# Performance work log

Measured on AMD Instinct MI355X. Metric: run time of the kernel, lower is better.

## Reference

```python
import jax, jax.numpy as jnp
import numpy as np

COST_CLASS = 1.0
COST_BBOX = 5.0
COST_GIOU = 2.0
EPS = 1e-7


def box_cxcywh_to_xyxy(x):
    cx, cy, w, h = x[..., 0], x[..., 1], x[..., 2], x[..., 3]
    return jnp.stack([cx - 0.5 * w, cy - 0.5 * h, cx + 0.5 * w, cy + 0.5 * h], axis=-1)


def generalized_box_iou(boxes1, boxes2):
    # boxes1: [N,4] xyxy, boxes2: [M,4] xyxy -> [N,M]
    area1 = (boxes1[:, 2] - boxes1[:, 0]) * (boxes1[:, 3] - boxes1[:, 1])
    area2 = (boxes2[:, 2] - boxes2[:, 0]) * (boxes2[:, 3] - boxes2[:, 1])
    lt = jnp.maximum(boxes1[:, None, :2], boxes2[None, :, :2])
    rb = jnp.minimum(boxes1[:, None, 2:], boxes2[None, :, 2:])
    wh = jnp.clip(rb - lt, 0.0)
    inter = wh[..., 0] * wh[..., 1]
    union = area1[:, None] + area2[None, :] - inter
    iou = inter / (union + EPS)
    # smallest enclosing box
    lt_c = jnp.minimum(boxes1[:, None, :2], boxes2[None, :, :2])
    rb_c = jnp.maximum(boxes1[:, None, 2:], boxes2[None, :, 2:])
    wh_c = jnp.clip(rb_c - lt_c, 0.0)
    c_area = wh_c[..., 0] * wh_c[..., 1]
    return iou - (c_area - union) / (c_area + EPS)


def setup_inputs() -> dict:
    key = jax.random.key(0)
    k1, k2, k3, k4 = jax.random.split(key, 4)
    bs, nq, nc, nt = 16, 900, 256, 800
    pred_logits = jax.random.normal(k1, (bs, nq, nc), dtype=jnp.float32)
    pred_boxes = jax.random.uniform(k2, (bs, nq, 4), dtype=jnp.float32)
    tgt_labels = jax.random.randint(k3, (nt,), 0, nc, dtype=jnp.int64)
    tgt_boxes = jax.random.uniform(k4, (nt, 4), dtype=jnp.float32)
    return {"pred_logits": pred_logits, "pred_boxes": pred_boxes,
            "tgt_labels": tgt_labels, "tgt_boxes": tgt_boxes}


def reference(pred_logits, pred_boxes, tgt_labels, tgt_boxes):
    # Returns the full pairwise matching cost tensor C: [bs, num_queries, total_targets].
    # (The scipy linear_sum_assignment / CPU Hungarian step consumes this on host.)
    bs, nq, nc = pred_logits.shape
    out_prob = jax.nn.softmax(pred_logits.reshape(bs * nq, nc), axis=-1)  # [N, nc]
    out_bbox = pred_boxes.reshape(bs * nq, 4)                              # [N, 4]
    cost_class = -out_prob[:, tgt_labels]                                  # [N, M]
    cost_bbox = jnp.abs(out_bbox[:, None, :] - tgt_boxes[None, :, :]).sum(-1)  # L1 cdist [N, M]
    cost_giou = -generalized_box_iou(box_cxcywh_to_xyxy(out_bbox),
                                     box_cxcywh_to_xyxy(tgt_boxes))        # [N, M]
    C = COST_BBOX * cost_bbox + COST_CLASS * cost_class + COST_GIOU * cost_giou
    return C.reshape(bs, nq, -1)
```

## Files before the change

kernel.cpp:

```cpp
#include <hip/hip_runtime.h>
#include <hip/hip_bf16.h>


constexpr float EPS = 1e-7f;

__device__ __forceinline__ float pair_cost(
    const float4& pb, float ax1, float ay1, float ax2, float ay2, float area1,
    const float4& tb, float prob)
{
    const float l1 = fabsf(pb.x - tb.x) + fabsf(pb.y - tb.y)
                   + fabsf(pb.z - tb.z) + fabsf(pb.w - tb.w);

    const float bx1 = tb.x - 0.5f * tb.z, by1 = tb.y - 0.5f * tb.w;
    const float bx2 = tb.x + 0.5f * tb.z, by2 = tb.y + 0.5f * tb.w;
    const float area2 = tb.z * tb.w;

    const float iw = fmaxf(fminf(ax2, bx2) - fmaxf(ax1, bx1), 0.0f);
    const float ih = fmaxf(fminf(ay2, by2) - fmaxf(ay1, by1), 0.0f);
    const float inter = iw * ih;
    const float uni   = area1 + area2 - inter;
    const float iou   = inter * __builtin_amdgcn_rcpf(uni + EPS);

    const float cw = fmaxf(ax2, bx2) - fminf(ax1, bx1);
    const float ch = fmaxf(ay2, by2) - fminf(ay1, by1);
    const float carea = cw * ch;

    const float giou = iou - (carea - uni) * __builtin_amdgcn_rcpf(carea + EPS);
    return 5.0f * l1 - prob - 2.0f * giou;
}

__global__ __launch_bounds__(256) void matcher_opt(
    const float* __restrict__ logits,
    const float* __restrict__ pboxes,
    const int*   __restrict__ labels,
    const float* __restrict__ tboxes,
    float* __restrict__ out,
    int N)
{
    const int wave = threadIdx.x >> 6;
    const int lane = threadIdx.x & 63;

    __shared__ float4 s_tb[800];
    __shared__ int    s_lb[800];
    __shared__ float  s_prob[4][256];

    for (int i = threadIdx.x; i < 800; i += 256) {
        s_tb[i] = reinterpret_cast<const float4*>(tboxes)[i];
        s_lb[i] = labels[i] & 255;
    }
    __syncthreads();

    float* sp = s_prob[wave];

    const int n0 = (blockIdx.x * 4 + wave) * 4;
    #pragma unroll 1
    for (int r = 0; r < 4; ++r) {
        const int n = n0 + r;
        if (n >= N) return;

        const float4 lg =
            reinterpret_cast<const float4*>(logits)[(size_t)n * 64 + lane];
        float mx = fmaxf(fmaxf(lg.x, lg.y), fmaxf(lg.z, lg.w));
        #pragma unroll
        for (int off = 32; off > 0; off >>= 1)
            mx = fmaxf(mx, __shfl_xor(mx, off, 64));
        const float e0 = __expf(lg.x - mx), e1 = __expf(lg.y - mx);
        const float e2 = __expf(lg.z - mx), e3 = __expf(lg.w - mx);
        float s = (e0 + e1) + (e2 + e3);
        #pragma unroll
        for (int off = 32; off > 0; off >>= 1)
            s += __shfl_xor(s, off, 64);
        const float inv = __builtin_amdgcn_rcpf(s);
        reinterpret_cast<float4*>(sp)[lane] =
            make_float4(e0 * inv, e1 * inv, e2 * inv, e3 * inv);

        const float4 pb = reinterpret_cast<const float4*>(pboxes)[n];
        const float ax1 = pb.x - 0.5f * pb.z, ay1 = pb.y - 0.5f * pb.w;
        const float ax2 = pb.x + 0.5f * pb.z, ay2 = pb.y + 0.5f * pb.w;
        const float area1 = pb.z * pb.w;

        float* orow = out + (size_t)n * 800;

        #pragma unroll 4
        for (int m = lane; m < 768; m += 64) {
            const float4 tb = s_tb[m];
            orow[m] = pair_cost(pb, ax1, ay1, ax2, ay2, area1, tb, sp[s_lb[m]]);
        }
        if (lane < 32) {
            const int m = 768 + lane;
            orow[m] = pair_cost(pb, ax1, ay1, ax2, ay2, area1, s_tb[m],
                                sp[s_lb[m]]);
        }
    }
}

__global__ __launch_bounds__(256) void matcher_generic(
    const float* __restrict__ logits, const float* __restrict__ pboxes,
    const int* __restrict__ labels, const float* __restrict__ tboxes,
    float* __restrict__ out, int N, int M, int NC, int lbl_mask)
{
    const int wave = threadIdx.x >> 6;
    const int lane = threadIdx.x & 63;
    const int n    = blockIdx.x * 4 + wave;

    extern __shared__ float s_dyn[];
    float* sp = s_dyn + wave * NC;

    if (n < N) {
        float mx = -3.4e38f;
        for (int c = lane; c < NC; c += 64) mx = fmaxf(mx, logits[(size_t)n * NC + c]);
        #pragma unroll
        for (int off = 32; off > 0; off >>= 1) mx = fmaxf(mx, __shfl_xor(mx, off, 64));
        float s = 0.f;
        for (int c = lane; c < NC; c += 64) {
            const float e = __expf(logits[(size_t)n * NC + c] - mx);
            sp[c] = e; s += e;
        }
        #pragma unroll
        for (int off = 32; off > 0; off >>= 1) s += __shfl_xor(s, off, 64);
        const float inv = __builtin_amdgcn_rcpf(s);
        for (int c = lane; c < NC; c += 64) sp[c] *= inv;
    }
    __syncthreads();
    if (n >= N) return;

    const float4 pb = reinterpret_cast<const float4*>(pboxes)[n];
    const float ax1 = pb.x - 0.5f * pb.z, ay1 = pb.y - 0.5f * pb.w;
    const float ax2 = pb.x + 0.5f * pb.z, ay2 = pb.y + 0.5f * pb.w;
    const float area1 = pb.z * pb.w;
    float* orow = out + (size_t)n * M;

    for (int m = lane; m < M; m += 64) {
        const float4 tb = reinterpret_cast<const float4*>(tboxes)[m];
        orow[m] = pair_cost(pb, ax1, ay1, ax2, ay2, area1, tb,
                            sp[labels[m] & lbl_mask]);
    }
}

extern "C" void kernel_launch(void* const* d_in, const int* in_sizes, int n_in,
                              void* d_out, int out_size, void* d_ws, size_t ws_size,
                              hipStream_t stream) {
    const float* logits = (const float*)d_in[0];
    const float* pboxes = (const float*)d_in[1];
    const int*   labels = (const int*)d_in[2];
    const float* tboxes = (const float*)d_in[3];

    const int N  = in_sizes[1] / 4;
    const int M  = in_sizes[2];
    const int NC = in_sizes[0] / N;

    if (NC == 256 && M == 800) {
        const int waves = (N + 3) / 4;
        const int grid  = (waves + 3) / 4;
        matcher_opt<<<grid, 256, 0, stream>>>(
            logits, pboxes, labels, tboxes, (float*)d_out, N);
    } else {
        int lbl_mask = 1; while (lbl_mask < NC) lbl_mask <<= 1;
        --lbl_mask;
        const int grid = (N + 3) / 4;
        matcher_generic<<<grid, 256, 4 * NC * sizeof(float), stream>>>(
            logits, pboxes, labels, tboxes, (float*)d_out, N, M, NC, lbl_mask);
    }
}
```

Measured before the change: 93.46 us.

## Process two query rows per wave with shared target-box preprocessing and nontemporal stores

Each wave now handles two query rows together instead of looping over four rows. Target-box corner and area values are computed once and reused for both rows, and the two softmax reductions are interleaved. Logits and prediction boxes are loaded before the shared-memory fill so the global load latency overlaps it. Output is written with nontemporal stores and the grid is doubled, which means more blocks each repeat the 800-entry target table load into shared memory.

```diff
diff --git a/kernel.cpp b/kernel.cpp
--- a/kernel.cpp
+++ b/kernel.cpp
@@ -4,16 +4,13 @@
 
 constexpr float EPS = 1e-7f;
 
-__device__ __forceinline__ float pair_cost(
+__device__ __forceinline__ float pair_cost_pp(
     const float4& pb, float ax1, float ay1, float ax2, float ay2, float area1,
-    const float4& tb, float prob)
+    const float4& tb, float bx1, float by1, float bx2, float by2, float area2,
+    float prob)
 {
     const float l1 = fabsf(pb.x - tb.x) + fabsf(pb.y - tb.y)
                    + fabsf(pb.z - tb.z) + fabsf(pb.w - tb.w);
-
-    const float bx1 = tb.x - 0.5f * tb.z, by1 = tb.y - 0.5f * tb.w;
-    const float bx2 = tb.x + 0.5f * tb.z, by2 = tb.y + 0.5f * tb.w;
-    const float area2 = tb.z * tb.w;
 
     const float iw = fmaxf(fminf(ax2, bx2) - fmaxf(ax1, bx1), 0.0f);
     const float ih = fmaxf(fminf(ay2, by2) - fmaxf(ay1, by1), 0.0f);
@@ -42,55 +39,98 @@
 
     __shared__ float4 s_tb[800];
     __shared__ int    s_lb[800];
-    __shared__ float  s_prob[4][256];
+    __shared__ float  s_prob[8][256];
+
+    const int n0 = (blockIdx.x * 4 + wave) * 2;
+    const int n1 = n0 + 1;
+    const bool v0 = n0 < N;
+    const bool v1 = n1 < N;
+
+    float4 lg0 = make_float4(0, 0, 0, 0), lg1 = lg0;
+    float4 pb0 = make_float4(0, 0, 0, 0), pb1 = pb0;
+    if (v0) {
+        lg0 = reinterpret_cast<const float4*>(logits)[(size_t)n0 * 64 + lane];
+        pb0 = reinterpret_cast<const float4*>(pboxes)[n0];
+    }
+    if (v1) {
+        lg1 = reinterpret_cast<const float4*>(logits)[(size_t)n1 * 64 + lane];
+        pb1 = reinterpret_cast<const float4*>(pboxes)[n1];
+    }
 
     for (int i = threadIdx.x; i < 800; i += 256) {
         s_tb[i] = reinterpret_cast<const float4*>(tboxes)[i];
         s_lb[i] = labels[i] & 255;
     }
     __syncthreads();
-
-    float* sp = s_prob[wave];
-
-    const int n0 = (blockIdx.x * 4 + wave) * 4;
-    #pragma unroll 1
-    for (int r = 0; r < 4; ++r) {
-        const int n = n0 + r;
-        if (n >= N) return;
-
-        const float4 lg =
-            reinterpret_cast<const float4*>(logits)[(size_t)n * 64 + lane];
-        float mx = fmaxf(fmaxf(lg.x, lg.y), fmaxf(lg.z, lg.w));
-        #pragma unroll
-        for (int off = 32; off > 0; off >>= 1)
-            mx = fmaxf(mx, __shfl_xor(mx, off, 64));
-        const float e0 = __expf(lg.x - mx), e1 = __expf(lg.y - mx);
-        const float e2 = __expf(lg.z - mx), e3 = __expf(lg.w - mx);
-        float s = (e0 + e1) + (e2 + e3);
-        #pragma unroll
-        for (int off = 32; off > 0; off >>= 1)
-            s += __shfl_xor(s, off, 64);
-        const float inv = __builtin_amdgcn_rcpf(s);
-        reinterpret_cast<float4*>(sp)[lane] =
-            make_float4(e0 * inv, e1 * inv, e2 * inv, e3 * inv);
-
-        const float4 pb = reinterpret_cast<const float4*>(pboxes)[n];
-        const float ax1 = pb.x - 0.5f * pb.z, ay1 = pb.y - 0.5f * pb.w;
-        const float ax2 = pb.x + 0.5f * pb.z, ay2 = pb.y + 0.5f * pb.w;
-        const float area1 = pb.z * pb.w;
-
-        float* orow = out + (size_t)n * 800;
-
-        #pragma unroll 4
-        for (int m = lane; m < 768; m += 64) {
-            const float4 tb = s_tb[m];
-            orow[m] = pair_cost(pb, ax1, ay1, ax2, ay2, area1, tb, sp[s_lb[m]]);
-        }
-        if (lane < 32) {
-            const int m = 768 + lane;
-            orow[m] = pair_cost(pb, ax1, ay1, ax2, ay2, area1, s_tb[m],
-                                sp[s_lb[m]]);
-        }
+    if (!v0) return;
+    if (!v1) { lg1 = lg0; pb1 = pb0; }
+
+    float mx0 = fmaxf(fmaxf(lg0.x, lg0.y), fmaxf(lg0.z, lg0.w));
+    float mx1 = fmaxf(fmaxf(lg1.x, lg1.y), fmaxf(lg1.z, lg1.w));
+    #pragma unroll
+    for (int off = 32; off > 0; off >>= 1) {
+        mx0 = fmaxf(mx0, __shfl_xor(mx0, off, 64));
+        mx1 = fmaxf(mx1, __shfl_xor(mx1, off, 64));
+    }
+    const float e00 = __expf(lg0.x - mx0), e01 = __expf(lg0.y - mx0);
+    const float e02 = __expf(lg0.z - mx0), e03 = __expf(lg0.w - mx0);
+    const float e10 = __expf(lg1.x - mx1), e11 = __expf(lg1.y - mx1);
+    const float e12 = __expf(lg1.z - mx1), e13 = __expf(lg1.w - mx1);
+    float s0 = (e00 + e01) + (e02 + e03);
+    float s1 = (e10 + e11) + (e12 + e13);
+    #pragma unroll
+    for (int off = 32; off > 0; off >>= 1) {
+        s0 += __shfl_xor(s0, off, 64);
+        s1 += __shfl_xor(s1, off, 64);
+    }
+    const float inv0 = __builtin_amdgcn_rcpf(s0);
+    const float inv1 = __builtin_amdgcn_rcpf(s1);
+    float* sp0 = s_prob[wave * 2 + 0];
+    float* sp1 = s_prob[wave * 2 + 1];
+    reinterpret_cast<float4*>(sp0)[lane] =
+        make_float4(e00 * inv0, e01 * inv0, e02 * inv0, e03 * inv0);
+    reinterpret_cast<float4*>(sp1)[lane] =
+        make_float4(e10 * inv1, e11 * inv1, e12 * inv1, e13 * inv1);
+
+    const float ax10 = pb0.x - 0.5f * pb0.z, ay10 = pb0.y - 0.5f * pb0.w;
+    const float ax20 = pb0.x + 0.5f * pb0.z, ay20 = pb0.y + 0.5f * pb0.w;
+    const float area10 = pb0.z * pb0.w;
+    const float ax11 = pb1.x - 0.5f * pb1.z, ay11 = pb1.y - 0.5f * pb1.w;
+    const float ax21 = pb1.x + 0.5f * pb1.z, ay21 = pb1.y + 0.5f * pb1.w;
+    const float area11 = pb1.z * pb1.w;
+
+    float* orow0 = out + (size_t)n0 * 800;
+    float* orow1 = v1 ? out + (size_t)n1 * 800 : orow0;
+
+    #pragma unroll 2
+    for (int m = lane; m < 768; m += 64) {
+        const float4 tb = s_tb[m];
+        const int   lbl = s_lb[m];
+        const float p0  = sp0[lbl];
+        const float p1  = sp1[lbl];
+        const float bx1 = tb.x - 0.5f * tb.z, by1 = tb.y - 0.5f * tb.w;
+        const float bx2 = tb.x + 0.5f * tb.z, by2 = tb.y + 0.5f * tb.w;
+        const float area2 = tb.z * tb.w;
+        const float c0 = pair_cost_pp(pb0, ax10, ay10, ax20, ay20, area10,
+                                      tb, bx1, by1, bx2, by2, area2, p0);
+        const float c1 = pair_cost_pp(pb1, ax11, ay11, ax21, ay21, area11,
+                                      tb, bx1, by1, bx2, by2, area2, p1);
+        __builtin_nontemporal_store(c0, orow0 + m);
+        __builtin_nontemporal_store(c1, orow1 + m);
+    }
+    if (lane < 32) {
+        const int m = 768 + lane;
+        const float4 tb = s_tb[m];
+        const int   lbl = s_lb[m];
+        const float bx1 = tb.x - 0.5f * tb.z, by1 = tb.y - 0.5f * tb.w;
+        const float bx2 = tb.x + 0.5f * tb.z, by2 = tb.y + 0.5f * tb.w;
+        const float area2 = tb.z * tb.w;
+        const float c0 = pair_cost_pp(pb0, ax10, ay10, ax20, ay20, area10,
+                                      tb, bx1, by1, bx2, by2, area2, sp0[lbl]);
+        const float c1 = pair_cost_pp(pb1, ax11, ay11, ax21, ay21, area11,
+                                      tb, bx1, by1, bx2, by2, area2, sp1[lbl]);
+        __builtin_nontemporal_store(c0, orow0 + m);
+        __builtin_nontemporal_store(c1, orow1 + m);
     }
 }
 
@@ -132,8 +172,12 @@
 
     for (int m = lane; m < M; m += 64) {
         const float4 tb = reinterpret_cast<const float4*>(tboxes)[m];
-        orow[m] = pair_cost(pb, ax1, ay1, ax2, ay2, area1, tb,
-                            sp[labels[m] & lbl_mask]);
+        const float bx1 = tb.x - 0.5f * tb.z, by1 = tb.y - 0.5f * tb.w;
+        const float bx2 = tb.x + 0.5f * tb.z, by2 = tb.y + 0.5f * tb.w;
+        const float area2 = tb.z * tb.w;
+        orow[m] = pair_cost_pp(pb, ax1, ay1, ax2, ay2, area1,
+                               tb, bx1, by1, bx2, by2, area2,
+                               sp[labels[m] & lbl_mask]);
     }
 }
 
@@ -150,7 +194,7 @@
     const int NC = in_sizes[0] / N;
 
     if (NC == 256 && M == 800) {
-        const int waves = (N + 3) / 4;
+        const int waves = (N + 1) / 2;
         const int grid  = (waves + 3) / 4;
         matcher_opt<<<grid, 256, 0, stream>>>(
             logits, pboxes, labels, tboxes, (float*)d_out, N);
```

After: 91.37 us. -2.2%, faster.
